# Kernel tuning notes

Measured on AMD Instinct MI355X. Metric: run time of the kernel, lower is better.

The kernel has to match this reference:

```python
import jax, jax.numpy as jnp
import numpy as np

H = 64          # hidden_size
IN = 6          # input_size
PREDICT = 10    # predict_size


def _lstm_cell(x_t, h, c, Wih, Whh, bih, bhh):
    # PyTorch gate order: i, f, g, o ; gates = x W_ih^T + b_ih + h W_hh^T + b_hh
    g = x_t @ Wih.T + bih + h @ Whh.T + bhh            # [B, 4H]
    i, f, gg, o = jnp.split(g, 4, axis=-1)
    c_new = jax.nn.sigmoid(f) * c + jax.nn.sigmoid(i) * jnp.tanh(gg)
    h_new = jax.nn.sigmoid(o) * jnp.tanh(c_new)
    return h_new, c_new


def setup_inputs() -> dict:
    key = jax.random.key(0)
    ks = jax.random.split(key, 12)
    B, T = 4096, 1024
    s = 1.0 / np.sqrt(H)  # torch default uniform init bound
    u = lambda k, shape: jax.random.uniform(k, shape, jnp.float32, -s, s)
    return {
        "x": jax.random.normal(ks[0], (B, T, IN), jnp.float32),
        "W_ih0": u(ks[1], (4 * H, IN)),
        "W_hh0": u(ks[2], (4 * H, H)),
        "b_ih0": u(ks[3], (4 * H,)),
        "b_hh0": u(ks[4], (4 * H,)),
        "W_ih1": u(ks[5], (4 * H, H)),
        "W_hh1": u(ks[6], (4 * H, H)),
        "b_ih1": u(ks[7], (4 * H,)),
        "b_hh1": u(ks[8], (4 * H,)),
        "fc_w": u(ks[9], (IN, H)),
        "fc_b": u(ks[10], (IN,)),
    }


def reference(x, W_ih0, W_hh0, b_ih0, b_hh0, W_ih1, W_hh1, b_ih1, b_hh1, fc_w, fc_b):
    B = x.shape[0]
    zeros = jnp.zeros((B, H), x.dtype)
    init = (zeros, zeros, zeros, zeros)  # h0, c0, h1, c1

    def stacked_step(carry, x_t):
        h0, c0, h1, c1 = carry
        h0, c0 = _lstm_cell(x_t, h0, c0, W_ih0, W_hh0, b_ih0, b_hh0)
        h1, c1 = _lstm_cell(h0, h1, c1, W_ih1, W_hh1, b_ih1, b_hh1)
        return (h0, c0, h1, c1), None

    # Encoder: scan over time (batch_first -> transpose to [T, B, IN])
    carry, _ = jax.lax.scan(stacked_step, init, jnp.swapaxes(x, 0, 1))

    def dec_step(state, _):
        dec_in, c = state
        c, _ = stacked_step(c, dec_in)
        pred = c[0 + 2] @ fc_w.T + fc_b  # top-layer h -> [B, IN]
        return (pred, c), pred

    dec_in0 = x[:, -1, :]
    _, preds = jax.lax.scan(dec_step, (dec_in0, carry), None, length=PREDICT)
    return jnp.swapaxes(preds, 0, 1)  # [B, PREDICT, IN]
```

## Files before the change

### kernel.cpp

```cpp
#include <hip/hip_runtime.h>

#define T_SEQ   1024
#define INDIM   6
#define HDIM    64
#define NPRED   10
#define CHNK    128
#define S0      104
#define NROWS   16

typedef __bf16         bf16x8 __attribute__((ext_vector_type(8)));
typedef float          f32x4  __attribute__((ext_vector_type(4)));
typedef unsigned short us4    __attribute__((ext_vector_type(4)));

#define MFMA16(acc, a, b) (acc) = __builtin_amdgcn_mfma_f32_16x16x32_bf16((a), (b), (acc), 0, 0, 0)

static __device__ __forceinline__ float bf2f(unsigned short b) {
  union { unsigned int u; float f; } v; v.u = ((unsigned int)b) << 16; return v.f;
}
static __device__ __forceinline__ unsigned short f2bf(float f) {
  union { float f; unsigned int u; } v; v.f = f;
  unsigned int r = v.u + 0x7FFFu + ((v.u >> 16) & 1u);
  return (unsigned short)(r >> 16);
}
static __device__ __forceinline__ float sigf(float x) {
  return __builtin_amdgcn_rcpf(1.0f + __builtin_amdgcn_exp2f(x * -1.442695040888963f));
}
static __device__ __forceinline__ float tanh_f(float x) {
  return 2.0f * __builtin_amdgcn_rcpf(1.0f + __builtin_amdgcn_exp2f(x * -2.885390081777927f)) - 1.0f;
}

template <bool F32>
__global__ __launch_bounds__(512, 2)
void lstm2_pipe(const void* __restrict__ xv,
                const void* __restrict__ Wih0v,
                const void* __restrict__ Whh0v,
                const void* __restrict__ bih0v,
                const void* __restrict__ bhh0v,
                const void* __restrict__ Wih1v,
                const void* __restrict__ Whh1v,
                const void* __restrict__ bih1v,
                const void* __restrict__ bhh1v,
                const void* __restrict__ fcwv,
                const void* __restrict__ fcbv,
                void* __restrict__ outv)
{
  {
    const unsigned short* w0u = (const unsigned short*)Wih0v;
    int votes = 0;
#pragma unroll
    for (int i = 0; i < 16; ++i) {
      const unsigned e = (w0u[2 * i] >> 7) & 0xFF;
      votes += (e >= 0x80 || e <= 0x40) ? 1 : 0;
    }
    if ((votes >= 4) != F32) return;
  }

  __shared__ __align__(16) unsigned short A0[2][NROWS * S0];
  __shared__ __align__(16) unsigned short A1[2][NROWS * S0];
  __shared__ __align__(16) unsigned short XB[NROWS * CHNK * INDIM];
  __shared__ __align__(16) unsigned short FCW[INDIM * HDIM];
  __shared__ float FCB[INDIM];

  const int tid   = threadIdx.x;
  const int lane  = tid & 63;
  const int wave  = tid >> 6;
  const bool isA  = (wave < 4);
  const int  wv4  = wave & 3;
  const int  q    = lane >> 4;
  const int  n    = lane & 15;
  const int  u    = 16 * wv4 + n;
  const int rbase = blockIdx.x * NROWS;

  {
    unsigned short* p0 = &A0[0][0];
    unsigned short* p1 = &A1[0][0];
    for (int i = tid; i < 2 * NROWS * S0; i += 512) { p0[i] = 0; p1[i] = 0; }
  }
  for (int i = tid; i < INDIM * HDIM; i += 512) {
    if constexpr (F32) FCW[i] = f2bf(((const float*)fcwv)[i]);
    else               FCW[i] = ((const unsigned short*)fcwv)[i];
  }
  if (tid < INDIM) {
    if constexpr (F32) FCB[tid] = ((const float*)fcbv)[tid];
    else               FCB[tid] = bf2f(((const unsigned short*)fcbv)[tid]);
  }

  auto ld1 = [&](const void* p, int i) -> float {
    if constexpr (F32) return ((const float*)p)[i];
    else               return bf2f(((const unsigned short*)p)[i]);
  };
  auto ld8 = [&](const void* W, int off) -> bf16x8 {
    union { unsigned short us[8]; bf16x8 v; } t;
    if constexpr (F32) {
      const float* p = (const float*)W + off;
#pragma unroll
      for (int j = 0; j < 8; ++j) t.us[j] = f2bf(p[j]);
    } else {
      t.v = *(const bf16x8*)((const unsigned short*)W + off);
    }
    return t.v;
  };

  bf16x8 WA[12], WB[16];
  float bA[4], bB[4];
#pragma unroll
  for (int gt = 0; gt < 4; ++gt) {
    const int col = 64 * gt + u;
    WA[gt * 3 + 0] = ld8(Whh0v, col * HDIM + 8 * q);
    WA[gt * 3 + 1] = ld8(Whh0v, col * HDIM + 32 + 8 * q);
    union { unsigned short us[8]; bf16x8 v; } t2;
#pragma unroll
    for (int j = 0; j < 8; ++j) t2.us[j] = 0;
    if (q == 0) {
#pragma unroll
      for (int j = 0; j < INDIM; ++j) t2.us[j] = f2bf(ld1(Wih0v, col * INDIM + j));
    }
    WA[gt * 3 + 2] = t2.v;
    bA[gt] = ld1(bih0v, col) + ld1(bhh0v, col);

    WB[gt * 4 + 0] = ld8(Wih1v, col * HDIM + 8 * q);
    WB[gt * 4 + 1] = ld8(Wih1v, col * HDIM + 32 + 8 * q);
    WB[gt * 4 + 2] = ld8(Whh1v, col * HDIM + 8 * q);
    WB[gt * 4 + 3] = ld8(Whh1v, col * HDIM + 32 + 8 * q);
    bB[gt] = ld1(bih1v, col) + ld1(bhh1v, col);
  }

  auto load_chunk = [&](int t0c) {
    if constexpr (F32) {
      const char* xb = (const char*)xv;
      for (int c = tid; c < NROWS * 192; c += 512) {
        const int row = c / 192;
        const int off = c - row * 192;
        const float4 v = *(const float4*)(xb + (size_t)(rbase + row) * (T_SEQ * INDIM * 4)
                                             + (size_t)t0c * (INDIM * 4) + (size_t)off * 16);
        us4 o;
        o.x = f2bf(v.x); o.y = f2bf(v.y); o.z = f2bf(v.z); o.w = f2bf(v.w);
        *(us4*)((char*)XB + (size_t)c * 8) = o;
      }
    } else {
      const char* xb = (const char*)xv;
      for (int c = tid; c < NROWS * 96; c += 512) {
        const int row = c / 96;
        const int off = c - row * 96;
        const int4 v = *(const int4*)(xb + (size_t)(rbase + row) * (T_SEQ * INDIM * 2)
                                         + (size_t)t0c * (INDIM * 2) + (size_t)off * 16);
        *(int4*)((char*)XB + (size_t)c * 16) = v;
      }
    }
  };

  load_chunk(0);
  __syncthreads();

  const int xrow   = tid / INDIM;
  const int xk     = tid - xrow * INDIM;
  const int xWrOff = xrow * S0 + HDIM + xk;
  const int xbBase = xrow * (CHNK * INDIM) + xk;

  if (tid < 96) A0[0][xWrOff] = XB[xbBase];
  __syncthreads();

  const int aOff = n * S0 + 8 * q;
  const int hOff = (4 * q) * S0 + u;

  float cc[4] = {0.f, 0.f, 0.f, 0.f};

  int t0v = 0;
  for (int i = 0; i <= T_SEQ; ++i) {
    if (((i + 1) & (CHNK - 1)) == 0 && (i + 1) < T_SEQ) {
      load_chunk(i + 1);
      __syncthreads();
      t0v = i + 1;
    }
    const int cur = i & 1;
    const unsigned short* A0c = &A0[cur][0];
    unsigned short*       A0n = &A0[cur ^ 1][0];
    const unsigned short* A1c = &A1[cur][0];
    unsigned short*       A1n = &A1[cur ^ 1][0];

    if (isA) {
      if (i < T_SEQ) {
        const bf16x8 f0 = *(const bf16x8*)(A0c + aOff);
        const bf16x8 f1 = *(const bf16x8*)(A0c + aOff + 32);
        const bf16x8 f2 = *(const bf16x8*)(A0c + aOff + 64);
        f32x4 g0 = {bA[0], bA[0], bA[0], bA[0]};
        f32x4 g1 = {bA[1], bA[1], bA[1], bA[1]};
        f32x4 g2 = {bA[2], bA[2], bA[2], bA[2]};
        f32x4 g3 = {bA[3], bA[3], bA[3], bA[3]};
        MFMA16(g0, f0, WA[0]);  MFMA16(g0, f1, WA[1]);  MFMA16(g0, f2, WA[2]);
        MFMA16(g1, f0, WA[3]);  MFMA16(g1, f1, WA[4]);  MFMA16(g1, f2, WA[5]);
        MFMA16(g2, f0, WA[6]);  MFMA16(g2, f1, WA[7]);  MFMA16(g2, f2, WA[8]);
        MFMA16(g3, f0, WA[9]);  MFMA16(g3, f1, WA[10]); MFMA16(g3, f2, WA[11]);
#pragma unroll
        for (int r = 0; r < 4; ++r) {
          const float is = sigf(g0[r]);
          const float fs = sigf(g1[r]);
          const float gv = tanh_f(g2[r]);
          const float os = sigf(g3[r]);
          cc[r] = fs * cc[r] + is * gv;
          A0n[hOff + r * S0] = f2bf(os * tanh_f(cc[r]));
        }
        const int srct = (i + 1 < T_SEQ) ? (i + 1) : (T_SEQ - 1);
        if (tid < 96) A0n[xWrOff] = XB[xbBase + (srct - t0v) * INDIM];
      }
    } else {
      if (i >= 1) {
        const bf16x8 h0 = *(const bf16x8*)(A0c + aOff);
        const bf16x8 h1 = *(const bf16x8*)(A0c + aOff + 32);
        const bf16x8 r0 = *(const bf16x8*)(A1c + aOff);
        const bf16x8 r1 = *(const bf16x8*)(A1c + aOff + 32);
        f32x4 g0 = {bB[0], bB[0], bB[0], bB[0]};
        f32x4 g1 = {bB[1], bB[1], bB[1], bB[1]};
        f32x4 g2 = {bB[2], bB[2], bB[2], bB[2]};
        f32x4 g3 = {bB[3], bB[3], bB[3], bB[3]};
        MFMA16(g0, h0, WB[0]);  MFMA16(g0, h1, WB[1]);  MFMA16(g0, r0, WB[2]);  MFMA16(g0, r1, WB[3]);
        MFMA16(g1, h0, WB[4]);  MFMA16(g1, h1, WB[5]);  MFMA16(g1, r0, WB[6]);  MFMA16(g1, r1, WB[7]);
        MFMA16(g2, h0, WB[8]);  MFMA16(g2, h1, WB[9]);  MFMA16(g2, r0, WB[10]); MFMA16(g2, r1, WB[11]);
        MFMA16(g3, h0, WB[12]); MFMA16(g3, h1, WB[13]); MFMA16(g3, r0, WB[14]); MFMA16(g3, r1, WB[15]);
#pragma unroll
        for (int r = 0; r < 4; ++r) {
          const float is = sigf(g0[r]);
          const float fs = sigf(g1[r]);
          const float gv = tanh_f(g2[r]);
          const float os = sigf(g3[r]);
          cc[r] = fs * cc[r] + is * gv;
          A1n[hOff + r * S0] = f2bf(os * tanh_f(cc[r]));
        }
      }
    }
    __syncthreads();
  }

  unsigned short* H0 = &A0[0][0];
  unsigned short* H1 = &A1[1][0];
  for (int d = 0; d < NPRED; ++d) {
    bf16x8 fa0 = {}, fa1 = {}, fa2 = {}, fr0 = {}, fr1 = {};
    if (isA) {
      fa0 = *(const bf16x8*)(H0 + aOff);
      fa1 = *(const bf16x8*)(H0 + aOff + 32);
      fa2 = *(const bf16x8*)(H0 + aOff + 64);
    } else {
      fr0 = *(const bf16x8*)(H1 + aOff);
      fr1 = *(const bf16x8*)(H1 + aOff + 32);
    }
    __syncthreads();
    if (isA) {
      f32x4 g0 = {bA[0], bA[0], bA[0], bA[0]};
      f32x4 g1 = {bA[1], bA[1], bA[1], bA[1]};
      f32x4 g2 = {bA[2], bA[2], bA[2], bA[2]};
      f32x4 g3 = {bA[3], bA[3], bA[3], bA[3]};
      MFMA16(g0, fa0, WA[0]);  MFMA16(g0, fa1, WA[1]);  MFMA16(g0, fa2, WA[2]);
      MFMA16(g1, fa0, WA[3]);  MFMA16(g1, fa1, WA[4]);  MFMA16(g1, fa2, WA[5]);
      MFMA16(g2, fa0, WA[6]);  MFMA16(g2, fa1, WA[7]);  MFMA16(g2, fa2, WA[8]);
      MFMA16(g3, fa0, WA[9]);  MFMA16(g3, fa1, WA[10]); MFMA16(g3, fa2, WA[11]);
#pragma unroll
      for (int r = 0; r < 4; ++r) {
        const float is = sigf(g0[r]);
        const float fs = sigf(g1[r]);
        const float gv = tanh_f(g2[r]);
        const float os = sigf(g3[r]);
        cc[r] = fs * cc[r] + is * gv;
        H0[hOff + r * S0] = f2bf(os * tanh_f(cc[r]));
      }
    }
    __syncthreads();
    if (!isA) {
      const bf16x8 h0 = *(const bf16x8*)(H0 + aOff);
      const bf16x8 h1 = *(const bf16x8*)(H0 + aOff + 32);
      f32x4 g0 = {bB[0], bB[0], bB[0], bB[0]};
      f32x4 g1 = {bB[1], bB[1], bB[1], bB[1]};
      f32x4 g2 = {bB[2], bB[2], bB[2], bB[2]};
      f32x4 g3 = {bB[3], bB[3], bB[3], bB[3]};
      MFMA16(g0, h0, WB[0]);  MFMA16(g0, h1, WB[1]);  MFMA16(g0, fr0, WB[2]);  MFMA16(g0, fr1, WB[3]);
      MFMA16(g1, h0, WB[4]);  MFMA16(g1, h1, WB[5]);  MFMA16(g1, fr0, WB[6]);  MFMA16(g1, fr1, WB[7]);
      MFMA16(g2, h0, WB[8]);  MFMA16(g2, h1, WB[9]);  MFMA16(g2, fr0, WB[10]); MFMA16(g2, fr1, WB[11]);
      MFMA16(g3, h0, WB[12]); MFMA16(g3, h1, WB[13]); MFMA16(g3, fr0, WB[14]); MFMA16(g3, fr1, WB[15]);
#pragma unroll
      for (int r = 0; r < 4; ++r) {
        const float is = sigf(g0[r]);
        const float fs = sigf(g1[r]);
        const float gv = tanh_f(g2[r]);
        const float os = sigf(g3[r]);
        cc[r] = fs * cc[r] + is * gv;
        H1[hOff + r * S0] = f2bf(os * tanh_f(cc[r]));
      }
    }
    __syncthreads();
    if (tid < 96) {
      const unsigned short* h1row = H1 + xrow * S0;
      const int4* hp = (const int4*)h1row;
      const int4* wp = (const int4*)(&FCW[xk * HDIM]);
      float s = FCB[xk];
#pragma unroll
      for (int i8 = 0; i8 < 8; ++i8) {
        const int4 hv = hp[i8];
        const int4 wv2 = wp[i8];
        const unsigned int hu[4] = {(unsigned)hv.x, (unsigned)hv.y, (unsigned)hv.z, (unsigned)hv.w};
        const unsigned int wu[4] = {(unsigned)wv2.x, (unsigned)wv2.y, (unsigned)wv2.z, (unsigned)wv2.w};
#pragma unroll
        for (int k2 = 0; k2 < 4; ++k2) {
          union { unsigned int uu; float ff; } hl, hh2, wl, wh;
          hl.uu = hu[k2] << 16; hh2.uu = hu[k2] & 0xFFFF0000u;
          wl.uu = wu[k2] << 16; wh.uu  = wu[k2] & 0xFFFF0000u;
          s += hl.ff * wl.ff + hh2.ff * wh.ff;
        }
      }
      const unsigned short pb = f2bf(s);
      const size_t idx = (size_t)(rbase + xrow) * (NPRED * INDIM) + (size_t)d * INDIM + xk;
      if constexpr (F32) ((float*)outv)[idx] = s;
      else               ((unsigned short*)outv)[idx] = pb;
      H0[xWrOff] = pb;
    }
    __syncthreads();
  }
}

extern "C" void kernel_launch(void* const* d_in, const int* in_sizes, int n_in,
                              void* d_out, int out_size, void* d_ws, size_t ws_size,
                              hipStream_t stream) {
  (void)in_sizes; (void)n_in; (void)d_ws; (void)ws_size; (void)out_size;
  const void* x    = d_in[0];
  const void* Wih0 = d_in[1];
  const void* Whh0 = d_in[2];
  const void* bih0 = d_in[3];
  const void* bhh0 = d_in[4];
  const void* Wih1 = d_in[5];
  const void* Whh1 = d_in[6];
  const void* bih1 = d_in[7];
  const void* bhh1 = d_in[8];
  const void* fcw  = d_in[9];
  const void* fcb  = d_in[10];
  lstm2_pipe<true><<<dim3(4096 / NROWS), dim3(512), 0, stream>>>(
      x, Wih0, Whh0, bih0, bhh0, Wih1, Whh1, bih1, bhh1, fcw, fcb, d_out);
  lstm2_pipe<false><<<dim3(4096 / NROWS), dim3(512), 0, stream>>>(
      x, Wih0, Whh0, bih0, bhh0, Wih1, Whh1, bih1, bhh1, fcw, fcb, d_out);
}
```

Baseline: 1.050 ms.

## Split LSTM gate MFMA and activation into separate wave roles via LDS

Blocks grow to 1024 threads with four wave-group roles: two groups run the layer-0 and layer-1 gate MFMAs and write pre-activations to new LDS buffers G0/G1, and two groups read them and apply the sigmoid/tanh cell update. The goal is to shorten the per-step critical path by splitting matrix and transcendental work across waves. The cost is an extra LDS round trip and an extra barrier per timestep, plus roughly 40KB more shared memory, and occupancy falls to one block per CU. The x chunk size is also cut from 128 to 32 steps to fit the LDS budget, which means more chunk reloads and syncs.

After: 3.244 ms. +208.9%, slower.

```diff
diff --git a/kernel.cpp b/kernel.cpp
--- a/kernel.cpp
+++ b/kernel.cpp
@@ -4,15 +4,16 @@
 #define INDIM   6
 #define HDIM    64
 #define NPRED   10
-#define CHNK    128
+#define CHNK    32
 #define S0      104
 #define NROWS   16
+#define GSTR    20
 
 typedef __bf16         bf16x8 __attribute__((ext_vector_type(8)));
 typedef float          f32x4  __attribute__((ext_vector_type(4)));
 typedef unsigned short us4    __attribute__((ext_vector_type(4)));
 
-#define MFMA16(acc, a, b) (acc) = __builtin_amdgcn_mfma_f32_16x16x32_bf16((a), (b), (acc), 0, 0, 0)
+#define MFMA16(a, b, c) __builtin_amdgcn_mfma_f32_16x16x32_bf16((a), (b), (c), 0, 0, 0)
 
 static __device__ __forceinline__ float bf2f(unsigned short b) {
   union { unsigned int u; float f; } v; v.u = ((unsigned int)b) << 16; return v.f;
@@ -30,19 +31,19 @@
 }
 
 template <bool F32>
-__global__ __launch_bounds__(512, 2)
-void lstm2_pipe(const void* __restrict__ xv,
-                const void* __restrict__ Wih0v,
-                const void* __restrict__ Whh0v,
-                const void* __restrict__ bih0v,
-                const void* __restrict__ bhh0v,
-                const void* __restrict__ Wih1v,
-                const void* __restrict__ Whh1v,
-                const void* __restrict__ bih1v,
-                const void* __restrict__ bhh1v,
-                const void* __restrict__ fcwv,
-                const void* __restrict__ fcbv,
-                void* __restrict__ outv)
+__global__ __launch_bounds__(1024, 1)
+void lstm2_split(const void* __restrict__ xv,
+                 const void* __restrict__ Wih0v,
+                 const void* __restrict__ Whh0v,
+                 const void* __restrict__ bih0v,
+                 const void* __restrict__ bhh0v,
+                 const void* __restrict__ Wih1v,
+                 const void* __restrict__ Whh1v,
+                 const void* __restrict__ bih1v,
+                 const void* __restrict__ bhh1v,
+                 const void* __restrict__ fcwv,
+                 const void* __restrict__ fcbv,
+                 void* __restrict__ outv)
 {
   {
     const unsigned short* w0u = (const unsigned short*)Wih0v;
@@ -57,26 +58,28 @@
 
   __shared__ __align__(16) unsigned short A0[2][NROWS * S0];
   __shared__ __align__(16) unsigned short A1[2][NROWS * S0];
+  __shared__ __align__(16) float G0[4 * HDIM * GSTR];
+  __shared__ __align__(16) float G1[4 * HDIM * GSTR];
   __shared__ __align__(16) unsigned short XB[NROWS * CHNK * INDIM];
   __shared__ __align__(16) unsigned short FCW[INDIM * HDIM];
   __shared__ float FCB[INDIM];
 
-  const int tid   = threadIdx.x;
-  const int lane  = tid & 63;
-  const int wave  = tid >> 6;
-  const bool isA  = (wave < 4);
-  const int  wv4  = wave & 3;
-  const int  q    = lane >> 4;
-  const int  n    = lane & 15;
-  const int  u    = 16 * wv4 + n;
+  const int tid  = threadIdx.x;
+  const int lane = tid & 63;
+  const int wave = tid >> 6;
+  const int role = wave >> 2;
+  const int wv   = wave & 3;
+  const int q    = lane >> 4;
+  const int n    = lane & 15;
+  const int u    = 16 * wv + n;
   const int rbase = blockIdx.x * NROWS;
 
   {
     unsigned short* p0 = &A0[0][0];
     unsigned short* p1 = &A1[0][0];
-    for (int i = tid; i < 2 * NROWS * S0; i += 512) { p0[i] = 0; p1[i] = 0; }
-  }
-  for (int i = tid; i < INDIM * HDIM; i += 512) {
+    for (int i = tid; i < 2 * NROWS * S0; i += 1024) { p0[i] = 0; p1[i] = 0; }
+  }
+  for (int i = tid; i < INDIM * HDIM; i += 1024) {
     if constexpr (F32) FCW[i] = f2bf(((const float*)fcwv)[i]);
     else               FCW[i] = ((const unsigned short*)fcwv)[i];
   }
@@ -101,36 +104,44 @@
     return t.v;
   };
 
-  bf16x8 WA[12], WB[16];
-  float bA[4], bB[4];
-#pragma unroll
-  for (int gt = 0; gt < 4; ++gt) {
-    const int col = 64 * gt + u;
-    WA[gt * 3 + 0] = ld8(Whh0v, col * HDIM + 8 * q);
-    WA[gt * 3 + 1] = ld8(Whh0v, col * HDIM + 32 + 8 * q);
-    union { unsigned short us[8]; bf16x8 v; } t2;
-#pragma unroll
-    for (int j = 0; j < 8; ++j) t2.us[j] = 0;
-    if (q == 0) {
-#pragma unroll
-      for (int j = 0; j < INDIM; ++j) t2.us[j] = f2bf(ld1(Wih0v, col * INDIM + j));
-    }
-    WA[gt * 3 + 2] = t2.v;
-    bA[gt] = ld1(bih0v, col) + ld1(bhh0v, col);
-
-    WB[gt * 4 + 0] = ld8(Wih1v, col * HDIM + 8 * q);
-    WB[gt * 4 + 1] = ld8(Wih1v, col * HDIM + 32 + 8 * q);
-    WB[gt * 4 + 2] = ld8(Whh1v, col * HDIM + 8 * q);
-    WB[gt * 4 + 3] = ld8(Whh1v, col * HDIM + 32 + 8 * q);
-    bB[gt] = ld1(bih1v, col) + ld1(bhh1v, col);
+  bf16x8 WA[12]; f32x4 bvA[4];
+  bf16x8 WB[16]; f32x4 bvB[4];
+  if (role == 0) {
+#pragma unroll
+    for (int gt = 0; gt < 4; ++gt) {
+      const int col = 64 * gt + u;
+      WA[gt * 3 + 0] = ld8(Whh0v, col * HDIM + 8 * q);
+      WA[gt * 3 + 1] = ld8(Whh0v, col * HDIM + 32 + 8 * q);
+      union { unsigned short us[8]; bf16x8 v; } t2;
+#pragma unroll
+      for (int j = 0; j < 8; ++j) t2.us[j] = 0;
+      if (q == 0) {
+#pragma unroll
+        for (int j = 0; j < INDIM; ++j) t2.us[j] = f2bf(ld1(Wih0v, col * INDIM + j));
+      }
+      WA[gt * 3 + 2] = t2.v;
+      const float b = ld1(bih0v, col) + ld1(bhh0v, col);
+      bvA[gt] = (f32x4){b, b, b, b};
+    }
+  } else if (role == 1) {
+#pragma unroll
+    for (int gt = 0; gt < 4; ++gt) {
+      const int col = 64 * gt + u;
+      WB[gt * 4 + 0] = ld8(Wih1v, col * HDIM + 8 * q);
+      WB[gt * 4 + 1] = ld8(Wih1v, col * HDIM + 32 + 8 * q);
+      WB[gt * 4 + 2] = ld8(Whh1v, col * HDIM + 8 * q);
+      WB[gt * 4 + 3] = ld8(Whh1v, col * HDIM + 32 + 8 * q);
+      const float b = ld1(bih1v, col) + ld1(bhh1v, col);
+      bvB[gt] = (f32x4){b, b, b, b};
+    }
   }
 
   auto load_chunk = [&](int t0c) {
     if constexpr (F32) {
       const char* xb = (const char*)xv;
-      for (int c = tid; c < NROWS * 192; c += 512) {
-        const int row = c / 192;
-        const int off = c - row * 192;
+      for (int c = tid; c < NROWS * (CHNK * INDIM / 4); c += 1024) {
+        const int row = c / 48;
+        const int off = c - row * 48;
         const float4 v = *(const float4*)(xb + (size_t)(rbase + row) * (T_SEQ * INDIM * 4)
                                              + (size_t)t0c * (INDIM * 4) + (size_t)off * 16);
         us4 o;
@@ -139,9 +150,9 @@
       }
     } else {
       const char* xb = (const char*)xv;
-      for (int c = tid; c < NROWS * 96; c += 512) {
-        const int row = c / 96;
-        const int off = c - row * 96;
+      for (int c = tid; c < NROWS * (CHNK * INDIM / 8); c += 1024) {
+        const int row = c / 24;
+        const int off = c - row * 24;
         const int4 v = *(const int4*)(xb + (size_t)(rbase + row) * (T_SEQ * INDIM * 2)
                                          + (size_t)t0c * (INDIM * 2) + (size_t)off * 16);
         *(int4*)((char*)XB + (size_t)c * 16) = v;
@@ -152,16 +163,21 @@
   load_chunk(0);
   __syncthreads();
 
-  const int xrow   = tid / INDIM;
-  const int xk     = tid - xrow * INDIM;
-  const int xWrOff = xrow * S0 + HDIM + xk;
-  const int xbBase = xrow * (CHNK * INDIM) + xk;
-
-  if (tid < 96) A0[0][xWrOff] = XB[xbBase];
+  const int tid2   = tid - 512;
+  const bool xw    = (tid2 >= 0 && tid2 < NROWS * INDIM);
+  const int xrow2  = xw ? (tid2 / INDIM) : 0;
+  const int xk2    = xw ? (tid2 - xrow2 * INDIM) : 0;
+  const int xWrOff = xrow2 * S0 + HDIM + xk2;
+  const int xbBase = xrow2 * (CHNK * INDIM) + xk2;
+
+  if (xw) A0[0][xWrOff] = XB[xbBase];
   __syncthreads();
 
-  const int aOff = n * S0 + 8 * q;
-  const int hOff = (4 * q) * S0 + u;
+  const int aOff   = n * S0 + 8 * q;
+  const int gwBase = (16 * wv + n) * GSTR + 4 * q;
+  const int a      = wv;
+  const int grBase = lane * GSTR + 4 * a;
+  const int hBase  = 4 * a * S0 + lane;
 
   float cc[4] = {0.f, 0.f, 0.f, 0.f};
 
@@ -173,58 +189,73 @@
       t0v = i + 1;
     }
     const int cur = i & 1;
-    const unsigned short* A0c = &A0[cur][0];
-    unsigned short*       A0n = &A0[cur ^ 1][0];
-    const unsigned short* A1c = &A1[cur][0];
-    unsigned short*       A1n = &A1[cur ^ 1][0];
-
-    if (isA) {
+    if (role == 0) {
       if (i < T_SEQ) {
+        const unsigned short* A0c = &A0[cur][0];
         const bf16x8 f0 = *(const bf16x8*)(A0c + aOff);
         const bf16x8 f1 = *(const bf16x8*)(A0c + aOff + 32);
         const bf16x8 f2 = *(const bf16x8*)(A0c + aOff + 64);
-        f32x4 g0 = {bA[0], bA[0], bA[0], bA[0]};
-        f32x4 g1 = {bA[1], bA[1], bA[1], bA[1]};
-        f32x4 g2 = {bA[2], bA[2], bA[2], bA[2]};
-        f32x4 g3 = {bA[3], bA[3], bA[3], bA[3]};
-        MFMA16(g0, f0, WA[0]);  MFMA16(g0, f1, WA[1]);  MFMA16(g0, f2, WA[2]);
-        MFMA16(g1, f0, WA[3]);  MFMA16(g1, f1, WA[4]);  MFMA16(g1, f2, WA[5]);
-        MFMA16(g2, f0, WA[6]);  MFMA16(g2, f1, WA[7]);  MFMA16(g2, f2, WA[8]);
-        MFMA16(g3, f0, WA[9]);  MFMA16(g3, f1, WA[10]); MFMA16(g3, f2, WA[11]);
+#pragma unroll
+        for (int gt = 0; gt < 4; ++gt) {
+          f32x4 g = MFMA16(f0, WA[gt * 3 + 0], bvA[gt]);
+          g       = MFMA16(f1, WA[gt * 3 + 1], g);
+          g       = MFMA16(f2, WA[gt * 3 + 2], g);
+          *(f32x4*)&G0[gwBase + gt * (HDIM * GSTR)] = g;
+        }
+      }
+    } else if (role == 1) {
+      if (i >= 1) {
+        const unsigned short* A0c = &A0[cur][0];
+        const unsigned short* A1c = &A1[cur][0];
+        const bf16x8 h0a = *(const bf16x8*)(A0c + aOff);
+        const bf16x8 h0b = *(const bf16x8*)(A0c + aOff + 32);
+        const bf16x8 r0  = *(const bf16x8*)(A1c + aOff);
+        const bf16x8 r1  = *(const bf16x8*)(A1c + aOff + 32);
+#pragma unroll
+        for (int gt = 0; gt < 4; ++gt) {
+          f32x4 g = MFMA16(h0a, WB[gt * 4 + 0], bvB[gt]);
+          g       = MFMA16(h0b, WB[gt * 4 + 1], g);
+          g       = MFMA16(r0,  WB[gt * 4 + 2], g);
+          g       = MFMA16(r1,  WB[gt * 4 + 3], g);
+          *(f32x4*)&G1[gwBase + gt * (HDIM * GSTR)] = g;
+        }
+      }
+    }
+    __syncthreads();
+    if (role == 2) {
+      if (i < T_SEQ) {
+        const f32x4 gi = *(const f32x4*)&G0[grBase];
+        const f32x4 gf = *(const f32x4*)&G0[grBase + 1 * (HDIM * GSTR)];
+        const f32x4 gg = *(const f32x4*)&G0[grBase + 2 * (HDIM * GSTR)];
+        const f32x4 go = *(const f32x4*)&G0[grBase + 3 * (HDIM * GSTR)];
+        unsigned short* dst = &A0[cur ^ 1][0];
 #pragma unroll
         for (int r = 0; r < 4; ++r) {
-          const float is = sigf(g0[r]);
-          const float fs = sigf(g1[r]);
-          const float gv = tanh_f(g2[r]);
-          const float os = sigf(g3[r]);
+          const float is = sigf(gi[r]);
+          const float fs = sigf(gf[r]);
+          const float gv = tanh_f(gg[r]);
+          const float os = sigf(go[r]);
           cc[r] = fs * cc[r] + is * gv;
-          A0n[hOff + r * S0] = f2bf(os * tanh_f(cc[r]));
+          dst[hBase + r * S0] = f2bf(os * tanh_f(cc[r]));
         }
         const int srct = (i + 1 < T_SEQ) ? (i + 1) : (T_SEQ - 1);
-        if (tid < 96) A0n[xWrOff] = XB[xbBase + (srct - t0v) * INDIM];
-      }
-    } else {
+        if (xw) dst[xWrOff] = XB[xbBase + (srct - t0v) * INDIM];
+      }
+    } else if (role == 3) {
       if (i >= 1) {
-        const bf16x8 h0 = *(const bf16x8*)(A0c + aOff);
-        const bf16x8 h1 = *(const bf16x8*)(A0c + aOff + 32);
-        const bf16x8 r0 = *(const bf16x8*)(A1c + aOff);
-        const bf16x8 r1 = *(const bf16x8*)(A1c + aOff + 32);
-        f32x4 g0 = {bB[0], bB[0], bB[0], bB[0]};
-        f32x4 g1 = {bB[1], bB[1], bB[1], bB[1]};
-        f32x4 g2 = {bB[2], bB[2], bB[2], bB[2]};
-        f32x4 g3 = {bB[3], bB[3], bB[3], bB[3]};
-        MFMA16(g0, h0, WB[0]);  MFMA16(g0, h1, WB[1]);  MFMA16(g0, r0, WB[2]);  MFMA16(g0, r1, WB[3]);
-        MFMA16(g1, h0, WB[4]);  MFMA16(g1, h1, WB[5]);  MFMA16(g1, r0, WB[6]);  MFMA16(g1, r1, WB[7]);
-        MFMA16(g2, h0, WB[8]);  MFMA16(g2, h1, WB[9]);  MFMA16(g2, r0, WB[10]); MFMA16(g2, r1, WB[11]);
-        MFMA16(g3, h0, WB[12]); MFMA16(g3, h1, WB[13]); MFMA16(g3, r0, WB[14]); MFMA16(g3, r1, WB[15]);
+        const f32x4 gi = *(const f32x4*)&G1[grBase];
+        const f32x4 gf = *(const f32x4*)&G1[grBase + 1 * (HDIM * GSTR)];
+        const f32x4 gg = *(const f32x4*)&G1[grBase + 2 * (HDIM * GSTR)];
+        const f32x4 go = *(const f32x4*)&G1[grBase + 3 * (HDIM * GSTR)];
+        unsigned short* dst = &A1[cur ^ 1][0];
 #pragma unroll
         for (int r = 0; r < 4; ++r) {
-          const float is = sigf(g0[r]);
-          const float fs = sigf(g1[r]);
-          const float gv = tanh_f(g2[r]);
-          const float os = sigf(g3[r]);
+          const float is = sigf(gi[r]);
+          const float fs = sigf(gf[r]);
+          const float gv = tanh_f(gg[r]);
+          const float os = sigf(go[r]);
           cc[r] = fs * cc[r] + is * gv;
-          A1n[hOff + r * S0] = f2bf(os * tanh_f(cc[r]));
+          dst[hBase + r * S0] = f2bf(os * tanh_f(cc[r]));
         }
       }
     }
@@ -234,63 +265,71 @@
   unsigned short* H0 = &A0[0][0];
   unsigned short* H1 = &A1[1][0];
   for (int d = 0; d < NPRED; ++d) {
-    bf16x8 fa0 = {}, fa1 = {}, fa2 = {}, fr0 = {}, fr1 = {};
-    if (isA) {
-      fa0 = *(const bf16x8*)(H0 + aOff);
-      fa1 = *(const bf16x8*)(H0 + aOff + 32);
-      fa2 = *(const bf16x8*)(H0 + aOff + 64);
-    } else {
-      fr0 = *(const bf16x8*)(H1 + aOff);
-      fr1 = *(const bf16x8*)(H1 + aOff + 32);
-    }
-    __syncthreads();
-    if (isA) {
-      f32x4 g0 = {bA[0], bA[0], bA[0], bA[0]};
-      f32x4 g1 = {bA[1], bA[1], bA[1], bA[1]};
-      f32x4 g2 = {bA[2], bA[2], bA[2], bA[2]};
-      f32x4 g3 = {bA[3], bA[3], bA[3], bA[3]};
-      MFMA16(g0, fa0, WA[0]);  MFMA16(g0, fa1, WA[1]);  MFMA16(g0, fa2, WA[2]);
-      MFMA16(g1, fa0, WA[3]);  MFMA16(g1, fa1, WA[4]);  MFMA16(g1, fa2, WA[5]);
-      MFMA16(g2, fa0, WA[6]);  MFMA16(g2, fa1, WA[7]);  MFMA16(g2, fa2, WA[8]);
-      MFMA16(g3, fa0, WA[9]);  MFMA16(g3, fa1, WA[10]); MFMA16(g3, fa2, WA[11]);
+    if (role == 0) {
+      const bf16x8 f0 = *(const bf16x8*)(H0 + aOff);
+      const bf16x8 f1 = *(const bf16x8*)(H0 + aOff + 32);
+      const bf16x8 f2 = *(const bf16x8*)(H0 + aOff + 64);
+#pragma unroll
+      for (int gt = 0; gt < 4; ++gt) {
+        f32x4 g = MFMA16(f0, WA[gt * 3 + 0], bvA[gt]);
+        g       = MFMA16(f1, WA[gt * 3 + 1], g);
+        g       = MFMA16(f2, WA[gt * 3 + 2], g);
+        *(f32x4*)&G0[gwBase + gt * (HDIM * GSTR)] = g;
+      }
+    }
+    __syncthreads();
+    if (role == 2) {
+      const f32x4 gi = *(const f32x4*)&G0[grBase];
+      const f32x4 gf = *(const f32x4*)&G0[grBase + 1 * (HDIM * GSTR)];
+      const f32x4 gg = *(const f32x4*)&G0[grBase + 2 * (HDIM * GSTR)];
+      const f32x4 go = *(const f32x4*)&G0[grBase + 3 * (HDIM * GSTR)];
 #pragma unroll
       for (int r = 0; r < 4; ++r) {
-        const float is = sigf(g0[r]);
-        const float fs = sigf(g1[r]);
-        const float gv = tanh_f(g2[r]);
-        const float os = sigf(g3[r]);
+        const float is = sigf(gi[r]);
+        const float fs = sigf(gf[r]);
+        const float gv = tanh_f(gg[r]);
+        const float os = sigf(go[r]);
         cc[r] = fs * cc[r] + is * gv;
-        H0[hOff + r * S0] = f2bf(os * tanh_f(cc[r]));
-      }
-    }
-    __syncthreads();
-    if (!isA) {
-      const bf16x8 h0 = *(const bf16x8*)(H0 + aOff);
-      const bf16x8 h1 = *(const bf16x8*)(H0 + aOff + 32);
-      f32x4 g0 = {bB[0], bB[0], bB[0], bB[0]};
-      f32x4 g1 = {bB[1], bB[1], bB[1], bB[1]};
-      f32x4 g2 = {bB[2], bB[2], bB[2], bB[2]};
-      f32x4 g3 = {bB[3], bB[3], bB[3], bB[3]};
-      MFMA16(g0, h0, WB[0]);  MFMA16(g0, h1, WB[1]);  MFMA16(g0, fr0, WB[2]);  MFMA16(g0, fr1, WB[3]);
-      MFMA16(g1, h0, WB[4]);  MFMA16(g1, h1, WB[5]);  MFMA16(g1, fr0, WB[6]);  MFMA16(g1, fr1, WB[7]);
-      MFMA16(g2, h0, WB[8]);  MFMA16(g2, h1, WB[9]);  MFMA16(g2, fr0, WB[10]); MFMA16(g2, fr1, WB[11]);
-      MFMA16(g3, h0, WB[12]); MFMA16(g3, h1, WB[13]); MFMA16(g3, fr0, WB[14]); MFMA16(g3, fr1, WB[15]);
+        H0[hBase + r * S0] = f2bf(os * tanh_f(cc[r]));
+      }
+    }
+    __syncthreads();
+    if (role == 1) {
+      const bf16x8 h0a = *(const bf16x8*)(H0 + aOff);
+      const bf16x8 h0b = *(const bf16x8*)(H0 + aOff + 32);
+      const bf16x8 r0  = *(const bf16x8*)(H1 + aOff);
+      const bf16x8 r1  = *(const bf16x8*)(H1 + aOff + 32);
+#pragma unroll
+      for (int gt = 0; gt < 4; ++gt) {
+        f32x4 g = MFMA16(h0a, WB[gt * 4 + 0], bvB[gt]);
+        g       = MFMA16(h0b, WB[gt * 4 + 1], g);
+        g       = MFMA16(r0,  WB[gt * 4 + 2], g);
+        g       = MFMA16(r1,  WB[gt * 4 + 3], g);
+        *(f32x4*)&G1[gwBase + gt * (HDIM * GSTR)] = g;
+      }
+    }
+    __syncthreads();
+    if (role == 3) {
+      const f32x4 gi = *(const f32x4*)&G1[grBase];
+      const f32x4 gf = *(const f32x4*)&G1[grBase + 1 * (HDIM * GSTR)];
+      const f32x4 gg = *(const f32x4*)&G1[grBase + 2 * (HDIM * GSTR)];
+      const f32x4 go = *(const f32x4*)&G1[grBase + 3 * (HDIM * GSTR)];
 #pragma unroll
       for (int r = 0; r < 4; ++r) {
-        const float is = sigf(g0[r]);
-        const float fs = sigf(g1[r]);
-        const float gv = tanh_f(g2[r]);
-        const float os = sigf(g3[r]);
+        const float is = sigf(gi[r]);
+        const float fs = sigf(gf[r]);
+        const float gv = tanh_f(gg[r]);
+        const float os = sigf(go[r]);
         cc[r] = fs * cc[r] + is * gv;
-        H1[hOff + r * S0] = f2bf(os * tanh_f(cc[r]));
-      }
-    }
-    __syncthreads();
-    if (tid < 96) {
-      const unsigned short* h1row = H1 + xrow * S0;
+        H1[hBase + r * S0] = f2bf(os * tanh_f(cc[r]));
+      }
+    }
+    __syncthreads();
+    if (xw) {
+      const unsigned short* h1row = H1 + xrow2 * S0;
       const int4* hp = (const int4*)h1row;
-      const int4* wp = (const int4*)(&FCW[xk * HDIM]);
-      float s = FCB[xk];
+      const int4* wp = (const int4*)(&FCW[xk2 * HDIM]);
+      float s = FCB[xk2];
 #pragma unroll
       for (int i8 = 0; i8 < 8; ++i8) {
         const int4 hv = hp[i8];
@@ -306,7 +345,7 @@
         }
       }
       const unsigned short pb = f2bf(s);
-      const size_t idx = (size_t)(rbase + xrow) * (NPRED * INDIM) + (size_t)d * INDIM + xk;
+      const size_t idx = (size_t)(rbase + xrow2) * (NPRED * INDIM) + (size_t)d * INDIM + xk2;
       if constexpr (F32) ((float*)outv)[idx] = s;
       else               ((unsigned short*)outv)[idx] = pb;
       H0[xWrOff] = pb;
@@ -330,8 +369,8 @@
   const void* bhh1 = d_in[8];
   const void* fcw  = d_in[9];
   const void* fcb  = d_in[10];
-  lstm2_pipe<true><<<dim3(4096 / NROWS), dim3(512), 0, stream>>>(
+  lstm2_split<true><<<dim3(4096 / NROWS), dim3(1024), 0, stream>>>(
       x, Wih0, Whh0, bih0, bhh0, Wih1, Whh1, bih1, bhh1, fcw, fcb, d_out);
-  lstm2_pipe<false><<<dim3(4096 / NROWS), dim3(512), 0, stream>>>(
+  lstm2_split<false><<<dim3(4096 / NROWS), dim3(1024), 0, stream>>>(
       x, Wih0, Whh0, bih0, bhh0, Wih1, Whh1, bih1, bhh1, fcw, fcb, d_out);
 }
```
